# Optimization experiments

Measured on AMD Instinct MI355X. Metric: run time of the kernel, lower is better.

Reference implementation:

```python
import jax, jax.numpy as jnp
import numpy as np
import math

H = 1024   # num_heads (nodal_demands slice)
B0 = 64    # num_base_heads
F = 2048   # num_flows (diameter slice)
O = 2048   # num_outputs
N = 8192   # batch
NB = 6     # num_blocks


def _lin_params(key, fan_in, fan_out):
    kw, kb = jax.random.split(key)
    lim = 1.0 / math.sqrt(fan_in)
    W = jax.random.uniform(kw, (fan_out, fan_in), jnp.float32, -lim, lim)
    b = jax.random.uniform(kb, (fan_out,), jnp.float32, -lim, lim)
    return W, b


def setup_inputs() -> dict:
    key = jax.random.key(0)
    ks = jax.random.split(key, 12)
    x = jax.random.normal(ks[0], (N, H + B0 + F), jnp.float32)
    W_h0q, b_h0q = _lin_params(ks[1], B0, F)
    W_sq, b_sq = _lin_params(ks[2], H, F)
    W_h0h, b_h0h = _lin_params(ks[3], B0, H)
    W_S, b_S = _lin_params(ks[4], F, F)
    W_q0h, b_q0h = _lin_params(ks[5], F, H)
    W_out, b_out = _lin_params(ks[6], F, O)

    def stack(k, fan_in, fan_out):
        Ws, bs = zip(*[_lin_params(kk, fan_in, fan_out) for kk in jax.random.split(k, NB)])
        return jnp.stack(Ws), jnp.stack(bs)

    Wb_Aq, bb_Aq = stack(ks[7], F, F)
    Wb_Dh, bb_Dh = stack(ks[8], F, H)
    Wb_fh, bb_fh = stack(ks[9], F, H)
    Wb_hf, bb_hf = stack(ks[10], H, F)
    Wb_resq, bb_resq = stack(ks[11], F, H)
    a_hf = jnp.full((NB,), 0.25, jnp.float32)  # PReLU default init
    return {
        "x": x,
        "W_h0q": W_h0q, "b_h0q": b_h0q, "W_sq": W_sq, "b_sq": b_sq,
        "W_h0h": W_h0h, "b_h0h": b_h0h, "W_S": W_S, "b_S": b_S,
        "W_q0h": W_q0h, "b_q0h": b_q0h,
        "Wb_Aq": Wb_Aq, "bb_Aq": bb_Aq, "Wb_Dh": Wb_Dh, "bb_Dh": bb_Dh,
        "Wb_fh": Wb_fh, "bb_fh": bb_fh, "Wb_hf": Wb_hf, "bb_hf": bb_hf,
        "a_hf": a_hf, "Wb_resq": Wb_resq, "bb_resq": bb_resq,
        "W_out": W_out, "b_out": b_out,
    }


def _lin(x, W, b):
    return x @ W.T + b


def _forward(x, W_h0q, b_h0q, W_sq, b_sq, W_h0h, b_h0h, W_S, b_S,
             W_q0h, b_q0h, Wb_Aq, bb_Aq, Wb_Dh, bb_Dh, Wb_fh, bb_fh,
             Wb_hf, bb_hf, a_hf, Wb_resq, bb_resq, W_out, b_out):
    s = x[:, :H]              # nodal demands
    h0 = x[:, H:H + B0]       # base heads
    d = x[:, H + B0:]         # diameters; edge_features is the same slice
    res_h0_q = _lin(h0, W_h0q, b_h0q)                 # [N, F]
    res_s_q = _lin(s, W_sq, b_sq)                     # [N, F]
    res_h0_h = _lin(h0, W_h0h, b_h0h)                 # [N, H]
    res_S_q = jax.nn.relu(_lin(d, W_S, b_S))          # [N, F]
    q = (math.pi / 4.0) * jnp.square(d)               # [N, F]
    res_q_h = _lin(q, W_q0h, b_q0h)                   # [N, H]

    sum_q_const = res_s_q + res_h0_q                  # fused: reused every block
    sum_h_const = res_h0_h

    def block(carry, p):
        q, res_q_h = carry
        W_Aq, b_Aq, W_Dh, b_Dh, W_fh, b_fh, W_hf, b_hf, a, W_resq, b_resq = p
        A_q = _lin(q * res_S_q, W_Aq, b_Aq)                       # [N, F]
        D_h = jax.nn.relu(_lin(A_q, W_Dh, b_Dh))                  # [N, H]
        hid = A_q * (q + sum_q_const)                             # [N, F]
        h = jax.nn.relu(_lin(hid, W_fh, b_fh))                    # [N, H]
        z = _lin((h + sum_h_const + res_q_h) * D_h, W_hf, b_hf)   # [N, F]
        z = jnp.where(z >= 0, z, a * z)                           # PReLU (scalar a)
        q = q - z
        res_q_h = jax.nn.relu(_lin(q, W_resq, b_resq))
        return (q, res_q_h), None

    params = (Wb_Aq, bb_Aq, Wb_Dh, bb_Dh, Wb_fh, bb_fh, Wb_hf, bb_hf,
              a_hf, Wb_resq, bb_resq)
    (q, _), _ = jax.lax.scan(block, (q, res_q_h), params)
    return _lin(q, W_out, b_out)  # num_steps == 1 -> single prediction


def reference(x, W_h0q, b_h0q, W_sq, b_sq, W_h0h, b_h0h, W_S, b_S,
              W_q0h, b_q0h, Wb_Aq, bb_Aq, Wb_Dh, bb_Dh, Wb_fh, bb_fh,
              Wb_hf, bb_hf, a_hf, Wb_resq, bb_resq, W_out, b_out):
    return _forward(x, W_h0q, b_h0q, W_sq, b_sq, W_h0h, b_h0h, W_S, b_S,
                    W_q0h, b_q0h, Wb_Aq, bb_Aq, Wb_Dh, bb_Dh, Wb_fh, bb_fh,
                    Wb_hf, bb_hf, a_hf, Wb_resq, bb_resq, W_out, b_out)
```

## Files before the change

kernel.cpp:

```cpp
#include <hip/hip_runtime.h>
#include <cstdint>
#include <cstddef>

#define NS    8192
#define HDIM  1024
#define B0DIM 64
#define FDIM  2048
#define ODIM  2048
#define NBLK  6
#define XCOLS (HDIM + B0DIM + FDIM)
#define SBW   (HDIM + B0DIM)

typedef __bf16 bf16_t;
typedef __bf16 bf16x8 __attribute__((ext_vector_type(8)));
typedef float  f32x4  __attribute__((ext_vector_type(4)));

__device__ inline bf16x8 cvt8(f32x4 lo, f32x4 hi) {
  bf16x8 r;
#pragma unroll
  for (int i = 0; i < 4; ++i) { r[i] = (bf16_t)lo[i]; r[i + 4] = (bf16_t)hi[i]; }
  return r;
}

__device__ __forceinline__ void gload16(bf16_t* lds, const bf16_t* g) {
  __builtin_amdgcn_global_load_lds(
      (const __attribute__((address_space(1))) unsigned int*)g,
      (__attribute__((address_space(3))) unsigned int*)lds, 16, 0, 0);
}

__global__ __launch_bounds__(256) void prep(const float* __restrict__ x,
                                            bf16_t* __restrict__ xbf,
                                            bf16_t* __restrict__ dbf,
                                            bf16_t* __restrict__ qo) {
  int t = blockIdx.x * 256 + threadIdx.x;
  int n = t / 392;
  int c = t - n * 392;
  const float* p = x + (size_t)n * XCOLS + c * 8;
  f32x4 lo = *(const f32x4*)p;
  f32x4 hi = *(const f32x4*)(p + 4);
  if (c < 136) {
    *(bf16x8*)(xbf + (size_t)n * SBW + c * 8) = cvt8(lo, hi);
  } else {
    int j = c * 8 - SBW;
    bf16x8 od, oq;
#pragma unroll
    for (int i = 0; i < 4; ++i) {
      bf16_t b0 = (bf16_t)lo[i], b1 = (bf16_t)hi[i];
      od[i] = b0; od[i + 4] = b1;
      float f0 = (float)b0, f1 = (float)b1;
      oq[i]     = (bf16_t)(0.7853981633974483f * f0 * f0);
      oq[i + 4] = (bf16_t)(0.7853981633974483f * f1 * f1);
    }
    *(bf16x8*)(dbf + (size_t)n * FDIM + j) = od;
    *(bf16x8*)(qo  + (size_t)n * FDIM + j) = oq;
  }
}

__global__ __launch_bounds__(256) void wconv4(
    const float* __restrict__ s0, bf16_t* __restrict__ d0, int n0,
    const float* __restrict__ s1, bf16_t* __restrict__ d1, int n1,
    const float* __restrict__ s2, bf16_t* __restrict__ d2, int n2,
    const float* __restrict__ s3, bf16_t* __restrict__ d3, int n3) {
  int t = blockIdx.x * 256 + threadIdx.x;
  const float* s; bf16_t* d;
  if (t < n0) { s = s0 + (size_t)t * 8; d = d0 + (size_t)t * 8; }
  else {
    t -= n0;
    if (t < n1) { s = s1 + (size_t)t * 8; d = d1 + (size_t)t * 8; }
    else {
      t -= n1;
      if (t < n2) { s = s2 + (size_t)t * 8; d = d2 + (size_t)t * 8; }
      else {
        t -= n2;
        if (t < n3) { s = s3 + (size_t)t * 8; d = d3 + (size_t)t * 8; }
        else return;
      }
    }
  }
  f32x4 lo = *(const f32x4*)s, hi = *(const f32x4*)(s + 4);
  *(bf16x8*)d = cvt8(lo, hi);
}

template <int EPI>
__global__ __launch_bounds__(256) void gemm_bt(
    const bf16_t* __restrict__ A, int lda, const bf16_t* __restrict__ W, int K,
    const float* __restrict__ bias, bf16_t* __restrict__ C, int ldc,
    float* __restrict__ Cf, bf16_t* __restrict__ out2,
    const bf16_t* __restrict__ p1, const bf16_t* __restrict__ p2,
    const float* __restrict__ alpha_p) {
  __shared__ __align__(16) bf16_t As[128 * 32];
  __shared__ __align__(16) bf16_t Bs[128 * 32];

  const int tid  = threadIdx.x;
  const int lane = tid & 63;
  const int wave = tid >> 6;
  const int wm   = wave & 1;
  const int wn   = wave >> 1;
  const int row0 = blockIdx.y * 128;
  const int col0 = blockIdx.x * 128;

  const int srow = wave * 32 + (lane >> 2);
  const int scol = (lane & 3) * 8;
  const bf16_t* ga0 = A + (size_t)(row0 + srow) * lda + scol;
  const bf16_t* ga1 = ga0 + (size_t)16 * lda;
  const bf16_t* gb0 = W + (size_t)(col0 + srow) * K + scol;
  const bf16_t* gb1 = gb0 + (size_t)16 * K;
  bf16_t* la0 = &As[(wave * 32) * 32];
  bf16_t* la1 = &As[(wave * 32 + 16) * 32];
  bf16_t* lb0 = &Bs[(wave * 32) * 32];
  bf16_t* lb1 = &Bs[(wave * 32 + 16) * 32];

  f32x4 acc[4][4];
#pragma unroll
  for (int i = 0; i < 4; ++i)
#pragma unroll
    for (int j = 0; j < 4; ++j)
#pragma unroll
      for (int r = 0; r < 4; ++r) acc[i][j][r] = 0.0f;

  const int fr   = lane & 15;
  const int quad = lane >> 4;
  const int nk   = K >> 5;

  for (int kt = 0; kt < nk; ++kt) {
    const int ko = kt * 32;
    __syncthreads();
    gload16(la0, ga0 + ko);
    gload16(la1, ga1 + ko);
    gload16(lb0, gb0 + ko);
    gload16(lb1, gb1 + ko);
    __syncthreads();

    bf16x8 af[4], bfr[4];
#pragma unroll
    for (int mt = 0; mt < 4; ++mt)
      af[mt] = *(const bf16x8*)&As[(wm * 64 + mt * 16 + fr) * 32 + quad * 8];
#pragma unroll
    for (int nt = 0; nt < 4; ++nt)
      bfr[nt] = *(const bf16x8*)&Bs[(wn * 64 + nt * 16 + fr) * 32 + quad * 8];
#pragma unroll
    for (int mt = 0; mt < 4; ++mt)
#pragma unroll
      for (int nt = 0; nt < 4; ++nt)
        acc[mt][nt] = __builtin_amdgcn_mfma_f32_16x16x32_bf16(
            af[mt], bfr[nt], acc[mt][nt], 0, 0, 0);
  }

  float alpha = 0.0f;
  if (EPI == 5) alpha = (float)(bf16_t)alpha_p[0];

#pragma unroll
  for (int mt = 0; mt < 4; ++mt) {
#pragma unroll
    for (int nt = 0; nt < 4; ++nt) {
      int ccol = col0 + wn * 64 + nt * 16 + fr;
      float bv = (float)(bf16_t)bias[ccol];
#pragma unroll
      for (int r = 0; r < 4; ++r) {
        int crow = row0 + wm * 64 + mt * 16 + quad * 4 + r;
        size_t idx = (size_t)crow * ldc + ccol;
        float v = acc[mt][nt][r] + bv;
        if (EPI == 0) C[idx] = (bf16_t)v;
        if (EPI == 1) C[idx] = (bf16_t)(v > 0.0f ? v : 0.0f);
        if (EPI == 7) { v += (float)C[idx]; C[idx] = (bf16_t)v; }
        if (EPI == 2) {
          bf16_t rb = (bf16_t)(v > 0.0f ? v : 0.0f);
          C[idx] = rb;
          out2[idx] = (bf16_t)((float)rb * (float)p1[idx]);
        }
        if (EPI == 3) {
          bf16_t ab = (bf16_t)v;
          C[idx] = ab;
          out2[idx] = (bf16_t)((float)ab * ((float)p1[idx] + (float)p2[idx]));
        }
        if (EPI == 4) {
          bf16_t hb = (bf16_t)(v > 0.0f ? v : 0.0f);
          float dh = (float)C[idx];
          C[idx] = (bf16_t)(((float)hb + (float)p1[idx] + (float)p2[idx]) * dh);
        }
        if (EPI == 5) {
          float z = v >= 0.0f ? v : alpha * v;
          bf16_t qn = (bf16_t)((float)C[idx] - z);
          C[idx] = qn;
          out2[idx] = (bf16_t)((float)qn * (float)p1[idx]);
        }
        if (EPI == 6) Cf[idx] = v;
      }
    }
  }
}

template <int EPI>
static inline void launch_gemm(const bf16_t* A, int lda, const bf16_t* W, int K,
                               const float* bias, void* C, int M, bf16_t* out2,
                               const bf16_t* p1, const bf16_t* p2,
                               const float* alpha, hipStream_t s) {
  dim3 grid(M / 128, NS / 128), blk(256);
  gemm_bt<EPI><<<grid, blk, 0, s>>>(A, lda, W, K, bias, (bf16_t*)C, M,
                                    (float*)C, out2, p1, p2, alpha);
}

extern "C" void kernel_launch(void* const* d_in, const int* in_sizes, int n_in,
                              void* d_out, int out_size, void* d_ws,
                              size_t ws_size, hipStream_t stream) {
  const float* x      = (const float*)d_in[0];
  const float* W_h0q  = (const float*)d_in[1];
  const float* b_h0q  = (const float*)d_in[2];
  const float* W_sq   = (const float*)d_in[3];
  const float* b_sq   = (const float*)d_in[4];
  const float* W_h0h  = (const float*)d_in[5];
  const float* b_h0h  = (const float*)d_in[6];
  const float* W_S    = (const float*)d_in[7];
  const float* b_S    = (const float*)d_in[8];
  const float* W_q0h  = (const float*)d_in[9];
  const float* b_q0h  = (const float*)d_in[10];
  const float* Wb_Aq  = (const float*)d_in[11];
  const float* bb_Aq  = (const float*)d_in[12];
  const float* Wb_Dh  = (const float*)d_in[13];
  const float* bb_Dh  = (const float*)d_in[14];
  const float* Wb_fh  = (const float*)d_in[15];
  const float* bb_fh  = (const float*)d_in[16];
  const float* Wb_hf  = (const float*)d_in[17];
  const float* bb_hf  = (const float*)d_in[18];
  const float* a_hf   = (const float*)d_in[19];
  const float* Wb_rq  = (const float*)d_in[20];
  const float* bb_rq  = (const float*)d_in[21];
  const float* W_out  = (const float*)d_in[22];
  const float* b_out  = (const float*)d_in[23];

  const size_t NFb = (size_t)NS * FDIM * sizeof(bf16_t);
  const size_t NHb = (size_t)NS * HDIM * sizeof(bf16_t);
  if (ws_size < 4 * NFb + 4 * NHb) return;

  char* ws = (char*)d_ws;
  bf16_t* q     = (bf16_t*)(ws);
  bf16_t* resS  = (bf16_t*)(ws + NFb);
  bf16_t* sumq  = (bf16_t*)(ws + 2 * NFb);
  bf16_t* tF1   = (bf16_t*)(ws + 3 * NFb);
  bf16_t* resqh = (bf16_t*)(ws + 4 * NFb);
  bf16_t* sumh  = (bf16_t*)(ws + 4 * NFb + NHb);
  bf16_t* tH1   = (bf16_t*)(ws + 4 * NFb + 2 * NHb);
  bf16_t* WS    = (bf16_t*)(ws + 4 * NFb + 3 * NHb);
  bf16_t* xbf   = tH1;
  bf16_t* dbf   = sumq;
  bf16_t* AqB   = (bf16_t*)d_out;
  bf16_t* dW    = (bf16_t*)d_out + (size_t)NS * FDIM;
  bf16_t* tFh   = dW;

  const int uFF = FDIM * FDIM / 8;
  const int uHF = HDIM * FDIM / 8;
  const int uQ0 = FDIM * B0DIM / 8;
  const int uH0 = HDIM * B0DIM / 8;

  prep<<<NS * 392 / 256, 256, 0, stream>>>(x, xbf, dbf, q);

  wconv4<<<(uFF + 255) / 256, 256, 0, stream>>>(
      W_S, dW, uFF, nullptr, nullptr, 0, nullptr, nullptr, 0, nullptr, nullptr, 0);
  launch_gemm<2>(dbf, FDIM, dW, FDIM, b_S, resS, FDIM, tF1, q, nullptr, nullptr, stream);

  bf16_t* dWsq = dW;
  bf16_t* dWhq = dW + (size_t)uFF * 0 + (size_t)FDIM * HDIM;
  bf16_t* dWhh = dWhq + (size_t)FDIM * B0DIM;
  bf16_t* dWqh = dWhh + (size_t)HDIM * B0DIM;
  wconv4<<<(uHF + uQ0 + uH0 + uHF + 255) / 256, 256, 0, stream>>>(
      W_sq, dWsq, uHF, W_h0q, dWhq, uQ0, W_h0h, dWhh, uH0, W_q0h, dWqh, uHF);

  launch_gemm<0>(xbf, SBW, dWsq, HDIM, b_sq, sumq, FDIM, nullptr, nullptr, nullptr, nullptr, stream);
  launch_gemm<7>(xbf + HDIM, SBW, dWhq, B0DIM, b_h0q, sumq, FDIM, nullptr, nullptr, nullptr, nullptr, stream);
  launch_gemm<0>(xbf + HDIM, SBW, dWhh, B0DIM, b_h0h, sumh, HDIM, nullptr, nullptr, nullptr, nullptr, stream);
  launch_gemm<0>(q, FDIM, dWqh, FDIM, b_q0h, resqh, HDIM, nullptr, nullptr, nullptr, nullptr, stream);

  bf16_t* wA = WS;
  bf16_t* wD = WS + (size_t)FDIM * FDIM;
  bf16_t* wF = WS;
  bf16_t* wH = WS + (size_t)HDIM * FDIM;
  bf16_t* wR = WS + 2 * (size_t)HDIM * FDIM;

  for (int b = 0; b < NBLK; ++b) {
    const float* c_Aq = bb_Aq + (size_t)b * FDIM;
    const float* c_Dh = bb_Dh + (size_t)b * HDIM;
    const float* c_fh = bb_fh + (size_t)b * HDIM;
    const float* c_hf = bb_hf + (size_t)b * FDIM;
    const float* c_r  = bb_rq + (size_t)b * HDIM;

    wconv4<<<(uFF + uHF + 255) / 256, 256, 0, stream>>>(
        Wb_Aq + (size_t)b * FDIM * FDIM, wA, uFF,
        Wb_Dh + (size_t)b * HDIM * FDIM, wD, uHF,
        nullptr, nullptr, 0, nullptr, nullptr, 0);
    launch_gemm<3>(tF1, FDIM, wA, FDIM, c_Aq, AqB, FDIM, tFh, q, sumq, nullptr, stream);
    launch_gemm<1>(AqB, FDIM, wD, FDIM, c_Dh, tH1, HDIM, nullptr, nullptr, nullptr, nullptr, stream);

    wconv4<<<(3 * uHF + 255) / 256, 256, 0, stream>>>(
        Wb_fh + (size_t)b * HDIM * FDIM, wF, uHF,
        Wb_hf + (size_t)b * FDIM * HDIM, wH, uHF,
        Wb_rq + (size_t)b * HDIM * FDIM, wR, uHF,
        nullptr, nullptr, 0);
    launch_gemm<4>(tFh, FDIM, wF, FDIM, c_fh, tH1, HDIM, nullptr, sumh, resqh, nullptr, stream);
    launch_gemm<5>(tH1, HDIM, wH, HDIM, c_hf, q, FDIM, tF1, resS, nullptr, a_hf + b, stream);
    launch_gemm<1>(q, FDIM, wR, FDIM, c_r, resqh, HDIM, nullptr, nullptr, nullptr, nullptr, stream);
  }

  wconv4<<<(uFF + 255) / 256, 256, 0, stream>>>(
      W_out, WS, uFF, nullptr, nullptr, 0, nullptr, nullptr, 0, nullptr, nullptr, 0);
  launch_gemm<6>(q, FDIM, WS, FDIM, b_out, d_out, ODIM, nullptr, nullptr, nullptr, nullptr, stream);
}
```

Measured before the change: 3.549 ms.

## Triple-buffer LDS tiles in GEMM and add XCD-aware block swizzle

The GEMM main loop now keeps three LDS buffers for the A and B tiles and issues the async global-to-LDS loads two k-tiles ahead. A vmcnt wait plus one barrier per iteration replaces the two full __syncthreads, so memory latency overlaps the MFMA work. Workgroup IDs are also remapped so that blocks assigned round-robin to the same XCD cover contiguous output tiles, which should improve L2 reuse. The cost is three times the LDS footprint per block, which may lower occupancy. The swizzle assumes the total block count is a multiple of 8.

After: 2.943 ms. 1.21x faster.

```diff
diff --git a/kernel.cpp b/kernel.cpp
--- a/kernel.cpp
+++ b/kernel.cpp
@@ -88,16 +88,21 @@
     float* __restrict__ Cf, bf16_t* __restrict__ out2,
     const bf16_t* __restrict__ p1, const bf16_t* __restrict__ p2,
     const float* __restrict__ alpha_p) {
-  __shared__ __align__(16) bf16_t As[128 * 32];
-  __shared__ __align__(16) bf16_t Bs[128 * 32];
+  __shared__ __align__(16) bf16_t As[3][128 * 32];
+  __shared__ __align__(16) bf16_t Bs[3][128 * 32];
 
   const int tid  = threadIdx.x;
   const int lane = tid & 63;
   const int wave = tid >> 6;
   const int wm   = wave & 1;
   const int wn   = wave >> 1;
-  const int row0 = blockIdx.y * 128;
-  const int col0 = blockIdx.x * 128;
+
+  const int gx  = gridDim.x;
+  const int bid = blockIdx.y * gx + blockIdx.x;
+  const int cpx = (gx * gridDim.y) >> 3;
+  const int swz = (bid & 7) * cpx + (bid >> 3);
+  const int row0 = (swz / gx) * 128;
+  const int col0 = (swz % gx) * 128;
 
   const int srow = wave * 32 + (lane >> 2);
   const int scol = (lane & 3) * 8;
@@ -105,10 +110,8 @@
   const bf16_t* ga1 = ga0 + (size_t)16 * lda;
   const bf16_t* gb0 = W + (size_t)(col0 + srow) * K + scol;
   const bf16_t* gb1 = gb0 + (size_t)16 * K;
-  bf16_t* la0 = &As[(wave * 32) * 32];
-  bf16_t* la1 = &As[(wave * 32 + 16) * 32];
-  bf16_t* lb0 = &Bs[(wave * 32) * 32];
-  bf16_t* lb1 = &Bs[(wave * 32 + 16) * 32];
+  const int lofs0 = (wave * 32) * 32;
+  const int lofs1 = (wave * 32 + 16) * 32;
 
   f32x4 acc[4][4];
 #pragma unroll
@@ -122,29 +125,44 @@
   const int quad = lane >> 4;
   const int nk   = K >> 5;
 
-  for (int kt = 0; kt < nk; ++kt) {
-    const int ko = kt * 32;
-    __syncthreads();
-    gload16(la0, ga0 + ko);
-    gload16(la1, ga1 + ko);
-    gload16(lb0, gb0 + ko);
-    gload16(lb1, gb1 + ko);
-    __syncthreads();
-
+  auto stage = [&](int buf, int ko) {
+    gload16(&As[buf][lofs0], ga0 + ko);
+    gload16(&As[buf][lofs1], ga1 + ko);
+    gload16(&Bs[buf][lofs0], gb0 + ko);
+    gload16(&Bs[buf][lofs1], gb1 + ko);
+  };
+
+  auto compute = [&](int buf) {
     bf16x8 af[4], bfr[4];
 #pragma unroll
     for (int mt = 0; mt < 4; ++mt)
-      af[mt] = *(const bf16x8*)&As[(wm * 64 + mt * 16 + fr) * 32 + quad * 8];
+      af[mt] = *(const bf16x8*)&As[buf][(wm * 64 + mt * 16 + fr) * 32 + quad * 8];
 #pragma unroll
     for (int nt = 0; nt < 4; ++nt)
-      bfr[nt] = *(const bf16x8*)&Bs[(wn * 64 + nt * 16 + fr) * 32 + quad * 8];
+      bfr[nt] = *(const bf16x8*)&Bs[buf][(wn * 64 + nt * 16 + fr) * 32 + quad * 8];
 #pragma unroll
     for (int mt = 0; mt < 4; ++mt)
 #pragma unroll
       for (int nt = 0; nt < 4; ++nt)
         acc[mt][nt] = __builtin_amdgcn_mfma_f32_16x16x32_bf16(
             af[mt], bfr[nt], acc[mt][nt], 0, 0, 0);
-  }
+  };
+
+  stage(0, 0);
+  if (nk > 1) stage(1, 32);
+
+  int rd = 0, wr = 2;
+  for (int kt = 0; kt < nk - 1; ++kt) {
+    asm volatile("s_waitcnt vmcnt(4)" ::: "memory");
+    __builtin_amdgcn_s_barrier();
+    if (kt + 2 < nk) stage(wr, (kt + 2) * 32);
+    compute(rd);
+    rd = (rd == 2) ? 0 : rd + 1;
+    wr = (wr == 2) ? 0 : wr + 1;
+  }
+  asm volatile("s_waitcnt vmcnt(0)" ::: "memory");
+  __builtin_amdgcn_s_barrier();
+  compute(rd);
 
   float alpha = 0.0f;
   if (EPI == 5) alpha = (float)(bf16_t)alpha_p[0];
@@ -259,7 +277,7 @@
   launch_gemm<2>(dbf, FDIM, dW, FDIM, b_S, resS, FDIM, tF1, q, nullptr, nullptr, stream);
 
   bf16_t* dWsq = dW;
-  bf16_t* dWhq = dW + (size_t)uFF * 0 + (size_t)FDIM * HDIM;
+  bf16_t* dWhq = dW + (size_t)FDIM * HDIM;
   bf16_t* dWhh = dWhq + (size_t)FDIM * B0DIM;
   bf16_t* dWqh = dWhh + (size_t)HDIM * B0DIM;
   wconv4<<<(uHF + uQ0 + uH0 + uHF + 255) / 256, 256, 0, stream>>>(
```
